# Kernel optimization log

Hardware: AMD Instinct MI355X
Metric: run time of the kernel (lower is better)

## Reference

```python
import jax, jax.numpy as jnp
import numpy as np

HEADS = 8
DIM_HEAD = 64
SCALE = DIM_HEAD ** -0.5


def setup_inputs() -> dict:
    key = jax.random.key(0)
    ks = jax.random.split(key, 6)
    B, N, D = 1, 4096, 640
    INNER = HEADS * DIM_HEAD  # 512
    s = lambda fan_in: 1.0 / np.sqrt(fan_in)
    return {
        "x": jax.random.normal(ks[0], (B, N, D), dtype=jnp.float32),
        "Wq": jax.random.normal(ks[1], (D, INNER), dtype=jnp.float32) * s(D),
        "Wk": jax.random.normal(ks[2], (D, INNER), dtype=jnp.float32) * s(D),
        "Wv": jax.random.normal(ks[3], (D, INNER), dtype=jnp.float32) * s(D),
        "Wo": jax.random.normal(ks[4], (INNER, D), dtype=jnp.float32) * s(INNER),
        "bo": jnp.zeros((D,), dtype=jnp.float32),
    }


def reference(x, Wq, Wk, Wv, Wo, bo):
    B, N, _ = x.shape
    h, d = HEADS, DIM_HEAD
    # self-attention: context = x
    q = (x @ Wq).reshape(B, N, h, d).transpose(0, 2, 1, 3)  # [B,h,N,d]
    k = (x @ Wk).reshape(B, N, h, d).transpose(0, 2, 1, 3)
    v = (x @ Wv).reshape(B, N, h, d).transpose(0, 2, 1, 3)
    sim = jnp.einsum('bhid,bhjd->bhij', q, k) * SCALE  # [B,h,N,N]
    attn = jax.nn.softmax(sim, axis=-1)
    out = jnp.einsum('bhij,bhjd->bhid', attn, v)  # [B,h,N,d]
    out = out.transpose(0, 2, 1, 3).reshape(B, N, h * d)  # [B,N,inner]
    return out @ Wo + bo  # dropout p=0.0 is identity
```

## Files before the change

kernel.cpp:

```cpp
#include <hip/hip_runtime.h>
#include <math.h>

#define NSEQ   4096
#define DMODEL 640
#define NHEAD  8
#define DHEAD  64
#define INNER  512

typedef _Float16 f16;
typedef _Float16 f16x8 __attribute__((ext_vector_type(8)));
typedef _Float16 f16x4 __attribute__((ext_vector_type(4)));
typedef float    f32x4 __attribute__((ext_vector_type(4)));

#define MFMA16(a, b, c) __builtin_amdgcn_mfma_f32_16x16x32_f16((a), (b), (c), 0, 0, 0)

#define QSCALE 0.18033688011112042f

__device__ __forceinline__ void gl16(const f16* g, f16* l) {
    __builtin_amdgcn_global_load_lds(
        (const __attribute__((address_space(1))) unsigned int*)g,
        (__attribute__((address_space(3))) unsigned int*)l, 16, 0, 0);
}

__global__ __launch_bounds__(256) void cvt_x(const float* __restrict__ x,
                                             f16* __restrict__ xh) {
    int i = (blockIdx.x * 256 + threadIdx.x) * 8;
    float4 a = *(const float4*)&x[i];
    float4 b = *(const float4*)&x[i + 4];
    f16x8 o = {(f16)a.x, (f16)a.y, (f16)a.z, (f16)a.w,
               (f16)b.x, (f16)b.y, (f16)b.z, (f16)b.w};
    *(f16x8*)&xh[i] = o;
}

__global__ __launch_bounds__(256) void transpose_cvt(
    const float* __restrict__ src, f16* __restrict__ dst, int R, int C) {
    __shared__ __align__(16) f16 T[64][72];
    const int c0 = blockIdx.x * 64, r0 = blockIdx.y * 64;
    const int t = threadIdx.x;
    {
        int r = t >> 2, cb = (t & 3) * 16;
#pragma unroll
        for (int i = 0; i < 16; i += 4) {
            float4 v = *(const float4*)&src[(size_t)(r0 + r) * C + c0 + cb + i];
            T[cb + i + 0][r] = (f16)v.x;
            T[cb + i + 1][r] = (f16)v.y;
            T[cb + i + 2][r] = (f16)v.z;
            T[cb + i + 3][r] = (f16)v.w;
        }
    }
    __syncthreads();
    {
        int c = t >> 2, rb = (t & 3) * 16;
        f16* d = dst + (size_t)(c0 + c) * R + r0 + rb;
        *(f16x8*)d = *(const f16x8*)&T[c][rb];
        *(f16x8*)(d + 8) = *(const f16x8*)&T[c][rb + 8];
    }
}

__global__ __launch_bounds__(256) void qkv_gemm16(
    const f16* __restrict__ xh,
    const f16* __restrict__ WTq, const f16* __restrict__ WTk,
    const f16* __restrict__ WTv,
    f16* __restrict__ q16, f16* __restrict__ k16, f16* __restrict__ vT16)
{
    __shared__ __align__(16) f16 Xs[4096];
    __shared__ __align__(16) f16 Ws[4096];
    __shared__ __align__(16) f16 Cs[64][72];

    const int bx = blockIdx.x;
    const int by = blockIdx.y;
    const int bz = blockIdx.z;
    const f16* WT = (bz == 0) ? WTq : (bz == 1) ? WTk : WTv;

    const int tid = threadIdx.x;
    const int w = tid >> 6, lane = tid & 63;
    const int lr = lane & 15, lc = lane >> 4;
    const int srow8 = lane >> 3;
    const int le = 8 * ((lane & 7) ^ srow8);
    const int swz0 = 8 * (lc ^ (lr & 7));
    const int swz1 = 8 * ((lc + 4) ^ (lr & 7));
    const int m0 = by * 64, n0 = bx * 64;

    f32x4 acc[4] = {};

    for (int s = 0; s < DMODEL / 64; ++s) {
        const int k0 = s * 64;
#pragma unroll
        for (int c = 0; c < 2; ++c) {
            const int cc = w * 2 + c;
            gl16(xh + (size_t)(m0 + cc * 8 + srow8) * DMODEL + k0 + le,
                 &Xs[cc * 512]);
            gl16(WT + (size_t)(n0 + cc * 8 + srow8) * DMODEL + k0 + le,
                 &Ws[cc * 512]);
        }
        __syncthreads();
        f16x8 a0 = *(const f16x8*)&Xs[(16 * w + lr) * 64 + swz0];
        f16x8 a1 = *(const f16x8*)&Xs[(16 * w + lr) * 64 + swz1];
#pragma unroll
        for (int nt = 0; nt < 4; ++nt) {
            f16x8 b0 = *(const f16x8*)&Ws[(nt * 16 + lr) * 64 + swz0];
            f16x8 b1 = *(const f16x8*)&Ws[(nt * 16 + lr) * 64 + swz1];
            acc[nt] = MFMA16(a1, b1, MFMA16(a0, b0, acc[nt]));
        }
        __syncthreads();
    }

    const float sc = (bz == 0) ? QSCALE : 1.0f;
    if (bz < 2) {
#pragma unroll
        for (int nt = 0; nt < 4; ++nt)
#pragma unroll
            for (int r = 0; r < 4; ++r)
                Cs[16 * w + lc * 4 + r][nt * 16 + lr] = (f16)(acc[nt][r] * sc);
    } else {
#pragma unroll
        for (int nt = 0; nt < 4; ++nt)
#pragma unroll
            for (int r = 0; r < 4; ++r)
                Cs[nt * 16 + lr][16 * w + lc * 4 + r] = (f16)acc[nt][r];
    }
    __syncthreads();
    {
        const int rr = tid >> 2, cb = (tid & 3) * 16;
        f16x8 v0 = *(const f16x8*)&Cs[rr][cb];
        f16x8 v1 = *(const f16x8*)&Cs[rr][cb + 8];
        f16* dst;
        if (bz == 0)
            dst = q16 + ((size_t)bx * NSEQ + m0 + rr) * DHEAD + cb;
        else if (bz == 1)
            dst = k16 + ((size_t)bx * NSEQ + m0 + rr) * DHEAD + cb;
        else
            dst = vT16 + ((size_t)bx * DHEAD + rr) * NSEQ + m0 + cb;
        *(f16x8*)dst = v0;
        *(f16x8*)(dst + 8) = v1;
    }
}

__global__ __launch_bounds__(128) void attn_fwd(
    const f16* __restrict__ q16, const f16* __restrict__ k16,
    const f16* __restrict__ vT16, f16* __restrict__ aoh)
{
    __shared__ __align__(16) f16 KsB[2][4096];
    __shared__ __align__(16) f16 VtB[2][4096];
    __shared__ __align__(16) f16 Ps[32][72];

    const int qb = blockIdx.x;
    const int h  = blockIdx.y;
    const int tid = threadIdx.x;
    const int w = tid >> 6, lane = tid & 63;
    const int lr = lane & 15, lc = lane >> 4;
    const int srow8 = lane >> 3;
    const int le = 8 * ((lane & 7) ^ srow8);
    const int swz0 = 8 * (lc ^ (lr & 7));
    const int swz1 = 8 * ((lc + 4) ^ (lr & 7));

    const f16* kh = k16 + (size_t)h * NSEQ * DHEAD;
    const f16* vh = vT16 + (size_t)h * DHEAD * NSEQ;

    const f16* qp = q16 + ((size_t)h * NSEQ + qb * 32 + 16 * w + lr) * DHEAD;
    const f16x8 qf0 = *(const f16x8*)&qp[lc * 8];
    const f16x8 qf1 = *(const f16x8*)&qp[32 + lc * 8];

    float m_run = -INFINITY, l_run = 0.f;
    f32x4 o[4] = {};

#pragma unroll
    for (int c = 0; c < 4; ++c) {
        const int cc = w * 4 + c;
        gl16(kh + (size_t)cc * 512 + srow8 * 64 + le, &KsB[0][cc * 512]);
        gl16(vh + ((size_t)(cc * 8 + srow8)) * NSEQ + le, &VtB[0][cc * 512]);
    }
    __syncthreads();

    for (int kt = 0; kt < 64; ++kt) {
        const int cur = kt & 1;
        if (kt < 63) {
            const int nb = cur ^ 1;
#pragma unroll
            for (int c = 0; c < 4; ++c) {
                const int cc = w * 4 + c;
                gl16(kh + (size_t)(kt + 1) * 4096 + cc * 512 + srow8 * 64 + le,
                     &KsB[nb][cc * 512]);
                gl16(vh + ((size_t)(cc * 8 + srow8)) * NSEQ + (kt + 1) * 64 + le,
                     &VtB[nb][cc * 512]);
            }
        }

        f32x4 s[4];
        const f32x4 z4 = {0.f, 0.f, 0.f, 0.f};
#pragma unroll
        for (int t = 0; t < 4; ++t) {
            f16x8 ka = *(const f16x8*)&KsB[cur][(t * 16 + lr) * 64 + swz0];
            f16x8 kb = *(const f16x8*)&KsB[cur][(t * 16 + lr) * 64 + swz1];
            s[t] = MFMA16(kb, qf1, MFMA16(ka, qf0, z4));
        }

        float pm = s[0][0];
#pragma unroll
        for (int t = 0; t < 4; ++t)
#pragma unroll
            for (int r = 0; r < 4; ++r) pm = fmaxf(pm, s[t][r]);
        pm = fmaxf(pm, __shfl_xor(pm, 16));
        pm = fmaxf(pm, __shfl_xor(pm, 32));
        const float mn = fmaxf(m_run, pm);
        const float al = __builtin_amdgcn_exp2f(m_run - mn);
        m_run = mn;
        float p[4][4];
        float ps = 0.f;
#pragma unroll
        for (int t = 0; t < 4; ++t)
#pragma unroll
            for (int r = 0; r < 4; ++r) {
                p[t][r] = __builtin_amdgcn_exp2f(s[t][r] - mn);
                ps += p[t][r];
            }
        ps += __shfl_xor(ps, 16);
        ps += __shfl_xor(ps, 32);
        l_run = l_run * al + ps;

#pragma unroll
        for (int t = 0; t < 4; ++t) {
            f16x4 pk = {(f16)p[t][0], (f16)p[t][1], (f16)p[t][2], (f16)p[t][3]};
            *(f16x4*)&Ps[16 * w + lr][t * 16 + lc * 4] = pk;
        }

#pragma unroll
        for (int dt = 0; dt < 4; ++dt) o[dt] *= al;

        f16x8 pb0 = *(const f16x8*)&Ps[16 * w + lr][lc * 8];
        f16x8 pb1 = *(const f16x8*)&Ps[16 * w + lr][32 + lc * 8];
#pragma unroll
        for (int dt = 0; dt < 4; ++dt) {
            f16x8 va0 = *(const f16x8*)&VtB[cur][(dt * 16 + lr) * 64 + swz0];
            f16x8 va1 = *(const f16x8*)&VtB[cur][(dt * 16 + lr) * 64 + swz1];
            o[dt] = MFMA16(va1, pb1, MFMA16(va0, pb0, o[dt]));
        }
        __syncthreads();
    }

    const float linv = 1.0f / l_run;
    f16* dst = aoh + ((size_t)(qb * 32 + 16 * w + lr)) * INNER + h * DHEAD;
#pragma unroll
    for (int dt = 0; dt < 4; ++dt) {
        f16x4 ov = {(f16)(o[dt][0] * linv), (f16)(o[dt][1] * linv),
                    (f16)(o[dt][2] * linv), (f16)(o[dt][3] * linv)};
        *(f16x4*)&dst[dt * 16 + lc * 4] = ov;
    }
}

__global__ __launch_bounds__(256) void out_gemm16(
    const f16* __restrict__ A, const f16* __restrict__ WoT,
    const float* __restrict__ bias, float* __restrict__ C)
{
    __shared__ __align__(16) f16 Xs[4096];
    __shared__ __align__(16) f16 Ws[4096];

    const int bx = blockIdx.x;
    const int by = blockIdx.y;
    const int tid = threadIdx.x;
    const int w = tid >> 6, lane = tid & 63;
    const int lr = lane & 15, lc = lane >> 4;
    const int srow8 = lane >> 3;
    const int le = 8 * ((lane & 7) ^ srow8);
    const int swz0 = 8 * (lc ^ (lr & 7));
    const int swz1 = 8 * ((lc + 4) ^ (lr & 7));
    const int m0 = by * 64, n0 = bx * 64;

    f32x4 acc[4] = {};

    for (int s = 0; s < INNER / 64; ++s) {
        const int k0 = s * 64;
#pragma unroll
        for (int c = 0; c < 2; ++c) {
            const int cc = w * 2 + c;
            gl16(A + (size_t)(m0 + cc * 8 + srow8) * INNER + k0 + le,
                 &Xs[cc * 512]);
            gl16(WoT + (size_t)(n0 + cc * 8 + srow8) * INNER + k0 + le,
                 &Ws[cc * 512]);
        }
        __syncthreads();
        f16x8 a0 = *(const f16x8*)&Xs[(16 * w + lr) * 64 + swz0];
        f16x8 a1 = *(const f16x8*)&Xs[(16 * w + lr) * 64 + swz1];
#pragma unroll
        for (int nt = 0; nt < 4; ++nt) {
            f16x8 b0 = *(const f16x8*)&Ws[(nt * 16 + lr) * 64 + swz0];
            f16x8 b1 = *(const f16x8*)&Ws[(nt * 16 + lr) * 64 + swz1];
            acc[nt] = MFMA16(a1, b1, MFMA16(a0, b0, acc[nt]));
        }
        __syncthreads();
    }

#pragma unroll
    for (int nt = 0; nt < 4; ++nt) {
        const float b = bias[n0 + nt * 16 + lr];
#pragma unroll
        for (int r = 0; r < 4; ++r)
            C[(size_t)(m0 + 16 * w + lc * 4 + r) * DMODEL + n0 + nt * 16 + lr] =
                acc[nt][r] + b;
    }
}

extern "C" void kernel_launch(void* const* d_in, const int* in_sizes, int n_in,
                              void* d_out, int out_size, void* d_ws, size_t ws_size,
                              hipStream_t stream) {
    const float* x  = (const float*)d_in[0];
    const float* Wq = (const float*)d_in[1];
    const float* Wk = (const float*)d_in[2];
    const float* Wv = (const float*)d_in[3];
    const float* Wo = (const float*)d_in[4];
    const float* bo = (const float*)d_in[5];
    float* out = (float*)d_out;

    f16* xh  = (f16*)d_ws;
    f16* WTq = xh  + (size_t)NSEQ * DMODEL;
    f16* WTk = WTq + (size_t)INNER * DMODEL;
    f16* WTv = WTk + (size_t)INNER * DMODEL;
    f16* WoT = WTv + (size_t)INNER * DMODEL;
    f16* q16 = WoT + (size_t)DMODEL * INNER;
    f16* k16 = q16 + (size_t)NHEAD * NSEQ * DHEAD;
    f16* vT16 = k16 + (size_t)NHEAD * NSEQ * DHEAD;
    f16* aoh  = vT16 + (size_t)NHEAD * NSEQ * DHEAD;

    cvt_x<<<NSEQ * DMODEL / (256 * 8), 256, 0, stream>>>(x, xh);
    transpose_cvt<<<dim3(INNER / 64, DMODEL / 64), 256, 0, stream>>>(Wq, WTq, DMODEL, INNER);
    transpose_cvt<<<dim3(INNER / 64, DMODEL / 64), 256, 0, stream>>>(Wk, WTk, DMODEL, INNER);
    transpose_cvt<<<dim3(INNER / 64, DMODEL / 64), 256, 0, stream>>>(Wv, WTv, DMODEL, INNER);
    transpose_cvt<<<dim3(DMODEL / 64, INNER / 64), 256, 0, stream>>>(Wo, WoT, INNER, DMODEL);

    qkv_gemm16<<<dim3(NHEAD, NSEQ / 64, 3), 256, 0, stream>>>(
        xh, WTq, WTk, WTv, q16, k16, vT16);
    attn_fwd<<<dim3(NSEQ / 32, NHEAD), 128, 0, stream>>>(q16, k16, vT16, aoh);
    out_gemm16<<<dim3(DMODEL / 64, NSEQ / 64), 256, 0, stream>>>(aoh, WoT, bo, out);
}
```

Baseline: 202.4 us.

## Split attention KV range in two and merge partials inside output GEMM

The attention kernel now splits each head's key/value sequence into two halves across blocks, using 64-query blocks of four waves. Each block writes a normalized partial output plus its running max and sum. The output projection GEMM merges the two partials with log-sum-exp weights while staging A into shared memory. It also drops K/V double buffering, skips the rescale when no lane's max grows, swizzles the P tile, and fuses three weight transposes into one launch. The cost is extra partial-output traffic, a non-pipelined load in the out GEMM, and less overlap of global loads with compute in attention.

```diff
diff --git a/kernel.cpp b/kernel.cpp
--- a/kernel.cpp
+++ b/kernel.cpp
@@ -30,6 +30,36 @@
     f16x8 o = {(f16)a.x, (f16)a.y, (f16)a.z, (f16)a.w,
                (f16)b.x, (f16)b.y, (f16)b.z, (f16)b.w};
     *(f16x8*)&xh[i] = o;
+}
+
+__global__ __launch_bounds__(256) void transpose_cvt3(
+    const float* __restrict__ Wq, const float* __restrict__ Wk,
+    const float* __restrict__ Wv,
+    f16* __restrict__ WTq, f16* __restrict__ WTk, f16* __restrict__ WTv) {
+    __shared__ __align__(16) f16 T[64][72];
+    const float* src = blockIdx.z == 0 ? Wq : blockIdx.z == 1 ? Wk : Wv;
+    f16* dst = blockIdx.z == 0 ? WTq : blockIdx.z == 1 ? WTk : WTv;
+    const int R = DMODEL, C = INNER;
+    const int c0 = blockIdx.x * 64, r0 = blockIdx.y * 64;
+    const int t = threadIdx.x;
+    {
+        int r = t >> 2, cb = (t & 3) * 16;
+#pragma unroll
+        for (int i = 0; i < 16; i += 4) {
+            float4 v = *(const float4*)&src[(size_t)(r0 + r) * C + c0 + cb + i];
+            T[cb + i + 0][r] = (f16)v.x;
+            T[cb + i + 1][r] = (f16)v.y;
+            T[cb + i + 2][r] = (f16)v.z;
+            T[cb + i + 3][r] = (f16)v.w;
+        }
+    }
+    __syncthreads();
+    {
+        int c = t >> 2, rb = (t & 3) * 16;
+        f16* d = dst + (size_t)(c0 + c) * R + r0 + rb;
+        *(f16x8*)d = *(const f16x8*)&T[c][rb];
+        *(f16x8*)(d + 8) = *(const f16x8*)&T[c][rb + 8];
+    }
 }
 
 __global__ __launch_bounds__(256) void transpose_cvt(
@@ -136,16 +166,20 @@
     }
 }
 
-__global__ __launch_bounds__(128) void attn_fwd(
+__global__ __launch_bounds__(256, 4) void attn_fwd(
     const f16* __restrict__ q16, const f16* __restrict__ k16,
-    const f16* __restrict__ vT16, f16* __restrict__ aoh)
+    const f16* __restrict__ vT16, f16* __restrict__ Opart,
+    float* __restrict__ Ml)
 {
-    __shared__ __align__(16) f16 KsB[2][4096];
-    __shared__ __align__(16) f16 VtB[2][4096];
-    __shared__ __align__(16) f16 Ps[32][72];
-
-    const int qb = blockIdx.x;
-    const int h  = blockIdx.y;
+    __shared__ __align__(16) f16 Ks[4096];
+    __shared__ __align__(16) f16 Vt[4096];
+    __shared__ __align__(16) f16 Ps[4096];
+
+    const int lin = blockIdx.x + 64 * blockIdx.y + 512 * blockIdx.z;
+    const int h  = lin & 7;
+    const int qb = (lin >> 3) & 63;
+    const int sp = lin >> 9;
+
     const int tid = threadIdx.x;
     const int w = tid >> 6, lane = tid & 63;
     const int lr = lane & 15, lc = lane >> 4;
@@ -154,102 +188,100 @@
     const int swz0 = 8 * (lc ^ (lr & 7));
     const int swz1 = 8 * ((lc + 4) ^ (lr & 7));
 
-    const f16* kh = k16 + (size_t)h * NSEQ * DHEAD;
-    const f16* vh = vT16 + (size_t)h * DHEAD * NSEQ;
-
-    const f16* qp = q16 + ((size_t)h * NSEQ + qb * 32 + 16 * w + lr) * DHEAD;
+    const f16* kp = k16 + ((size_t)h * NSEQ + sp * 2048) * DHEAD;
+    const f16* vp = vT16 + (size_t)h * DHEAD * NSEQ + sp * 2048;
+
+    const f16* qp = q16 + ((size_t)h * NSEQ + qb * 64 + 16 * w + lr) * DHEAD;
     const f16x8 qf0 = *(const f16x8*)&qp[lc * 8];
     const f16x8 qf1 = *(const f16x8*)&qp[32 + lc * 8];
 
     float m_run = -INFINITY, l_run = 0.f;
     f32x4 o[4] = {};
 
-#pragma unroll
-    for (int c = 0; c < 4; ++c) {
-        const int cc = w * 4 + c;
-        gl16(kh + (size_t)cc * 512 + srow8 * 64 + le, &KsB[0][cc * 512]);
-        gl16(vh + ((size_t)(cc * 8 + srow8)) * NSEQ + le, &VtB[0][cc * 512]);
-    }
-    __syncthreads();
-
-    for (int kt = 0; kt < 64; ++kt) {
-        const int cur = kt & 1;
-        if (kt < 63) {
-            const int nb = cur ^ 1;
-#pragma unroll
-            for (int c = 0; c < 4; ++c) {
-                const int cc = w * 4 + c;
-                gl16(kh + (size_t)(kt + 1) * 4096 + cc * 512 + srow8 * 64 + le,
-                     &KsB[nb][cc * 512]);
-                gl16(vh + ((size_t)(cc * 8 + srow8)) * NSEQ + (kt + 1) * 64 + le,
-                     &VtB[nb][cc * 512]);
-            }
-        }
-
-        f32x4 s[4];
+    for (int kt = 0; kt < 32; ++kt) {
+#pragma unroll
+        for (int c = 0; c < 2; ++c) {
+            const int cc = 2 * w + c;
+            gl16(kp + (size_t)(kt * 64 + cc * 8 + srow8) * DHEAD + le,
+                 &Ks[cc * 512]);
+            gl16(vp + (size_t)(cc * 8 + srow8) * NSEQ + kt * 64 + le,
+                 &Vt[cc * 512]);
+        }
+        __syncthreads();
+
+        f32x4 sv[4];
         const f32x4 z4 = {0.f, 0.f, 0.f, 0.f};
 #pragma unroll
         for (int t = 0; t < 4; ++t) {
-            f16x8 ka = *(const f16x8*)&KsB[cur][(t * 16 + lr) * 64 + swz0];
-            f16x8 kb = *(const f16x8*)&KsB[cur][(t * 16 + lr) * 64 + swz1];
-            s[t] = MFMA16(kb, qf1, MFMA16(ka, qf0, z4));
-        }
-
-        float pm = s[0][0];
+            f16x8 ka = *(const f16x8*)&Ks[(t * 16 + lr) * 64 + swz0];
+            f16x8 kb = *(const f16x8*)&Ks[(t * 16 + lr) * 64 + swz1];
+            sv[t] = MFMA16(kb, qf1, MFMA16(ka, qf0, z4));
+        }
+
+        float pm = sv[0][0];
 #pragma unroll
         for (int t = 0; t < 4; ++t)
 #pragma unroll
-            for (int r = 0; r < 4; ++r) pm = fmaxf(pm, s[t][r]);
+            for (int r = 0; r < 4; ++r) pm = fmaxf(pm, sv[t][r]);
         pm = fmaxf(pm, __shfl_xor(pm, 16));
         pm = fmaxf(pm, __shfl_xor(pm, 32));
-        const float mn = fmaxf(m_run, pm);
-        const float al = __builtin_amdgcn_exp2f(m_run - mn);
-        m_run = mn;
+        if (__any(pm > m_run)) {
+            const float mn = fmaxf(m_run, pm);
+            const float al = __builtin_amdgcn_exp2f(m_run - mn);
+            m_run = mn;
+            l_run *= al;
+#pragma unroll
+            for (int dt = 0; dt < 4; ++dt) o[dt] *= al;
+        }
         float p[4][4];
         float ps = 0.f;
 #pragma unroll
         for (int t = 0; t < 4; ++t)
 #pragma unroll
             for (int r = 0; r < 4; ++r) {
-                p[t][r] = __builtin_amdgcn_exp2f(s[t][r] - mn);
+                p[t][r] = __builtin_amdgcn_exp2f(sv[t][r] - m_run);
                 ps += p[t][r];
             }
         ps += __shfl_xor(ps, 16);
         ps += __shfl_xor(ps, 32);
-        l_run = l_run * al + ps;
+        l_run += ps;
 
 #pragma unroll
         for (int t = 0; t < 4; ++t) {
             f16x4 pk = {(f16)p[t][0], (f16)p[t][1], (f16)p[t][2], (f16)p[t][3]};
-            *(f16x4*)&Ps[16 * w + lr][t * 16 + lc * 4] = pk;
-        }
-
-#pragma unroll
-        for (int dt = 0; dt < 4; ++dt) o[dt] *= al;
-
-        f16x8 pb0 = *(const f16x8*)&Ps[16 * w + lr][lc * 8];
-        f16x8 pb1 = *(const f16x8*)&Ps[16 * w + lr][32 + lc * 8];
+            const int col = (16 * t + 4 * lc) ^ ((lr & 7) << 3);
+            *(f16x4*)&Ps[(16 * w + lr) * 64 + col] = pk;
+        }
+
+        f16x8 pb0 = *(const f16x8*)&Ps[(16 * w + lr) * 64 + swz0];
+        f16x8 pb1 = *(const f16x8*)&Ps[(16 * w + lr) * 64 + swz1];
 #pragma unroll
         for (int dt = 0; dt < 4; ++dt) {
-            f16x8 va0 = *(const f16x8*)&VtB[cur][(dt * 16 + lr) * 64 + swz0];
-            f16x8 va1 = *(const f16x8*)&VtB[cur][(dt * 16 + lr) * 64 + swz1];
+            f16x8 va0 = *(const f16x8*)&Vt[(dt * 16 + lr) * 64 + swz0];
+            f16x8 va1 = *(const f16x8*)&Vt[(dt * 16 + lr) * 64 + swz1];
             o[dt] = MFMA16(va1, pb1, MFMA16(va0, pb0, o[dt]));
         }
         __syncthreads();
     }
 
     const float linv = 1.0f / l_run;
-    f16* dst = aoh + ((size_t)(qb * 32 + 16 * w + lr)) * INNER + h * DHEAD;
+    const size_t qg = (size_t)qb * 64 + 16 * w + lr;
+    f16* ob = Opart + (((size_t)(sp * 8 + h)) * NSEQ + qg) * DHEAD;
 #pragma unroll
     for (int dt = 0; dt < 4; ++dt) {
         f16x4 ov = {(f16)(o[dt][0] * linv), (f16)(o[dt][1] * linv),
                     (f16)(o[dt][2] * linv), (f16)(o[dt][3] * linv)};
-        *(f16x4*)&dst[dt * 16 + lc * 4] = ov;
+        *(f16x4*)&ob[dt * 16 + 4 * lc] = ov;
+    }
+    if (lc == 0) {
+        float2 ml = make_float2(m_run, l_run);
+        *(float2*)&Ml[(((size_t)(sp * 8 + h)) * NSEQ + qg) * 2] = ml;
     }
 }
 
 __global__ __launch_bounds__(256) void out_gemm16(
-    const f16* __restrict__ A, const f16* __restrict__ WoT,
+    const f16* __restrict__ Opart, const float* __restrict__ Ml,
+    const f16* __restrict__ WoT,
     const float* __restrict__ bias, float* __restrict__ C)
 {
     __shared__ __align__(16) f16 Xs[4096];
@@ -261,22 +293,37 @@
     const int w = tid >> 6, lane = tid & 63;
     const int lr = lane & 15, lc = lane >> 4;
     const int srow8 = lane >> 3;
-    const int le = 8 * ((lane & 7) ^ srow8);
+    const int j = lane & 7;
+    const int le = 8 * (j ^ srow8);
     const int swz0 = 8 * (lc ^ (lr & 7));
     const int swz1 = 8 * ((lc + 4) ^ (lr & 7));
     const int m0 = by * 64, n0 = bx * 64;
 
     f32x4 acc[4] = {};
 
-    for (int s = 0; s < INNER / 64; ++s) {
-        const int k0 = s * 64;
+    for (int s8 = 0; s8 < 8; ++s8) {
+        const int k0 = s8 * 64;
 #pragma unroll
         for (int c = 0; c < 2; ++c) {
             const int cc = w * 2 + c;
-            gl16(A + (size_t)(m0 + cc * 8 + srow8) * INNER + k0 + le,
-                 &Xs[cc * 512]);
             gl16(WoT + (size_t)(n0 + cc * 8 + srow8) * INNER + k0 + le,
                  &Ws[cc * 512]);
+            const int row = cc * 8 + srow8;
+            const size_t q = (size_t)m0 + row;
+            f16x8 o0 = *(const f16x8*)&Opart[((size_t)s8 * NSEQ + q) * DHEAD + 8 * j];
+            f16x8 o1 = *(const f16x8*)&Opart[((size_t)(8 + s8) * NSEQ + q) * DHEAD + 8 * j];
+            float2 ml0 = *(const float2*)&Ml[((size_t)s8 * NSEQ + q) * 2];
+            float2 ml1 = *(const float2*)&Ml[((size_t)(8 + s8) * NSEQ + q) * 2];
+            const float mx = fmaxf(ml0.x, ml1.x);
+            float w0 = ml0.y * __builtin_amdgcn_exp2f(ml0.x - mx);
+            float w1 = ml1.y * __builtin_amdgcn_exp2f(ml1.x - mx);
+            const float inv = 1.0f / (w0 + w1);
+            w0 *= inv; w1 *= inv;
+            f16x8 a8;
+#pragma unroll
+            for (int e = 0; e < 8; ++e)
+                a8[e] = (f16)((float)o0[e] * w0 + (float)o1[e] * w1);
+            *(f16x8*)&Xs[row * 64 + 8 * (j ^ (row & 7))] = a8;
         }
         __syncthreads();
         f16x8 a0 = *(const f16x8*)&Xs[(16 * w + lr) * 64 + swz0];
@@ -311,24 +358,28 @@
     const float* bo = (const float*)d_in[5];
     float* out = (float*)d_out;
 
-    f16* xh  = (f16*)d_ws;
-    f16* WTq = xh  + (size_t)NSEQ * DMODEL;
-    f16* WTk = WTq + (size_t)INNER * DMODEL;
-    f16* WTv = WTk + (size_t)INNER * DMODEL;
-    f16* WoT = WTv + (size_t)INNER * DMODEL;
-    f16* q16 = WoT + (size_t)DMODEL * INNER;
-    f16* k16 = q16 + (size_t)NHEAD * NSEQ * DHEAD;
-    f16* vT16 = k16 + (size_t)NHEAD * NSEQ * DHEAD;
-    f16* aoh  = vT16 + (size_t)NHEAD * NSEQ * DHEAD;
+    char* base = (char*)d_ws;
+    f16*   Opart = (f16*)base;
+    f16*   xh    = (f16*)base;
+    f16*   WTq   = xh + (size_t)NSEQ * DMODEL;
+    f16*   WTk   = WTq + (size_t)INNER * DMODEL;
+    f16*   WTv   = WTk + (size_t)INNER * DMODEL;
+    float* Ml    = (float*)(base + 8388608);
+    f16*   WoT   = (f16*)(base + 8912896);
+    f16*   q16   = (f16*)(base + 9568256);
+    f16*   k16   = q16 + (size_t)NHEAD * NSEQ * DHEAD;
+    f16*   vT16  = k16 + (size_t)NHEAD * NSEQ * DHEAD;
 
     cvt_x<<<NSEQ * DMODEL / (256 * 8), 256, 0, stream>>>(x, xh);
-    transpose_cvt<<<dim3(INNER / 64, DMODEL / 64), 256, 0, stream>>>(Wq, WTq, DMODEL, INNER);
-    transpose_cvt<<<dim3(INNER / 64, DMODEL / 64), 256, 0, stream>>>(Wk, WTk, DMODEL, INNER);
-    transpose_cvt<<<dim3(INNER / 64, DMODEL / 64), 256, 0, stream>>>(Wv, WTv, DMODEL, INNER);
-    transpose_cvt<<<dim3(DMODEL / 64, INNER / 64), 256, 0, stream>>>(Wo, WoT, INNER, DMODEL);
+    transpose_cvt3<<<dim3(INNER / 64, DMODEL / 64, 3), 256, 0, stream>>>(
+        Wq, Wk, Wv, WTq, WTk, WTv);
+    transpose_cvt<<<dim3(DMODEL / 64, INNER / 64), 256, 0, stream>>>(
+        Wo, WoT, INNER, DMODEL);
 
     qkv_gemm16<<<dim3(NHEAD, NSEQ / 64, 3), 256, 0, stream>>>(
         xh, WTq, WTk, WTv, q16, k16, vT16);
-    attn_fwd<<<dim3(NSEQ / 32, NHEAD), 128, 0, stream>>>(q16, k16, vT16, aoh);
-    out_gemm16<<<dim3(DMODEL / 64, NSEQ / 64), 256, 0, stream>>>(aoh, WoT, bo, out);
-}
+    attn_fwd<<<dim3(NSEQ / 64, NHEAD, 2), 256, 0, stream>>>(
+        q16, k16, vT16, Opart, Ml);
+    out_gemm16<<<dim3(DMODEL / 64, NSEQ / 64), 256, 0, stream>>>(
+        Opart, Ml, WoT, bo, out);
+}
```

Result: faster. 171.5 us (-15.3%).
